# Performance work log

Measured on AMD Instinct MI355X. Metric: run time of the kernel, lower is better.

Reference implementation:

```python
import jax, jax.numpy as jnp
import numpy as np

K = 20
EPS = 1e-5  # BatchNorm eps
SLOPE = 0.2  # LeakyReLU negative slope


def _lrelu(y):
    return jnp.where(y > 0, y, SLOPE * y)


def _knn_idx(x):
    # x: [B, C, N] -> idx [B, N, K] of nearest neighbors (largest of negative sq dist)
    inner = -2.0 * jnp.einsum('bcn,bcm->bnm', x, x)
    xx = jnp.sum(x * x, axis=1)  # [B, N]
    pd = -xx[:, :, None] - inner - xx[:, None, :]  # [B, N, N]
    return jax.lax.top_k(pd, K)[1]


def _graph_feature(x):
    # x: [B, C, N] -> [B, 2C, N, K] = cat(neighbor - center, center)
    idx = _knn_idx(x)
    xt = jnp.transpose(x, (0, 2, 1))  # [B, N, C]
    nb = jax.vmap(lambda f, i: f[i])(xt, idx)  # [B, N, K, C]
    ctr = xt[:, :, None, :]
    feat = jnp.concatenate([nb - ctr, jnp.broadcast_to(ctr, nb.shape)], axis=-1)
    return jnp.transpose(feat, (0, 3, 1, 2))


def _bn(y, p, ch_axis):
    g, b, m, v = p[0], p[1], p[2], p[3]
    shape = [1] * y.ndim
    shape[ch_axis] = -1
    scale = (g / jnp.sqrt(v + EPS)).reshape(shape)
    return (y - m.reshape(shape)) * scale + b.reshape(shape)


def _conv_block(x, w, bn):
    f = _graph_feature(x)  # [B, 2C_in, N, K]
    y = jnp.einsum('bcnk,oc->bonk', f, w)  # 1x1 conv, no bias
    y = _lrelu(_bn(y, bn, 1))
    return jnp.max(y, axis=-1)  # max over K neighbors -> [B, C_out, N]


def setup_inputs() -> dict:
    key = jax.random.key(0)
    ks = jax.random.split(key, 20)
    B, N = 8, 1024
    inp = {
        'x': jax.random.normal(ks[0], (B, 3, N), jnp.float32),
        'w0': jax.random.normal(ks[1], (64, 6), jnp.float32) * 0.1,
        'w1': jax.random.normal(ks[2], (64, 128), jnp.float32) * 0.1,
        'w2': jax.random.normal(ks[3], (128, 128), jnp.float32) * 0.1,
        'w3': jax.random.normal(ks[4], (256, 256), jnp.float32) * 0.1,
        'bn0': jax.random.uniform(ks[5], (4, 64), jnp.float32) + 0.1,
        'bn1': jax.random.uniform(ks[6], (4, 64), jnp.float32) + 0.1,
        'bn2': jax.random.uniform(ks[7], (4, 128), jnp.float32) + 0.1,
        'bn3': jax.random.uniform(ks[8], (4, 256), jnp.float32) + 0.1,
        'we': jax.random.normal(ks[9], (1024, 512), jnp.float32) * 0.05,
        'bne': jax.random.uniform(ks[10], (4, 1024), jnp.float32) + 0.1,
        'wf0': jax.random.normal(ks[11], (512, 2048), jnp.float32) * 0.02,
        'bnf0': jax.random.uniform(ks[12], (4, 512), jnp.float32) + 0.1,
        'wf1': jax.random.normal(ks[13], (256, 512), jnp.float32) * 0.05,
        'bnf1': jax.random.uniform(ks[14], (4, 256), jnp.float32) + 0.1,
        'wfin': jax.random.normal(ks[15], (64, 256), jnp.float32) * 0.05,
        'bfin': jax.random.normal(ks[16], (64,), jnp.float32) * 0.05,
    }
    return inp


def reference(x, w0, w1, w2, w3, bn0, bn1, bn2, bn3, we, bne, wf0, bnf0, wf1, bnf1, wfin, bfin):
    B = x.shape[0]
    x1 = _conv_block(x, w0, bn0)   # [B, 64, N]
    x2 = _conv_block(x1, w1, bn1)  # [B, 64, N]
    x3 = _conv_block(x2, w2, bn2)  # [B, 128, N]
    x4 = _conv_block(x3, w3, bn3)  # [B, 256, N]
    cat = jnp.concatenate([x1, x2, x3, x4], axis=1)  # [B, 512, N]
    e = _lrelu(_bn(jnp.einsum('bcn,oc->bon', cat, we), bne, 1))  # [B, 1024, N]
    p1 = jnp.max(e, axis=-1)
    p2 = jnp.mean(e, axis=-1)
    h = jnp.concatenate([p1, p2], axis=1)  # [B, 2048]
    h = _lrelu(_bn(h @ wf0.T, bnf0, 1))  # [B, 512]; dropout is eval-mode identity
    h = _lrelu(_bn(h @ wf1.T, bnf1, 1))  # [B, 256]
    return h @ wfin.T + bfin  # [B, 64]
```

## Files before the change

kernel.cpp:

```cpp
#include <hip/hip_runtime.h>
#include <math.h>

#define N_PTS 1024
#define BATCH 8
#define KNN 20
#define EPSB 1e-5f
#define SLOPE 0.2f

typedef __attribute__((ext_vector_type(8))) short short8;
typedef __attribute__((ext_vector_type(4))) float f32x4;
typedef unsigned short ushort_t;
typedef unsigned long long u64;

#define LDS_U32(p) ((__attribute__((address_space(3))) unsigned int*)(p))
#define GLB_U32(p) ((const __attribute__((address_space(1))) unsigned int*)(p))

__device__ __forceinline__ void glds16(const ushort_t* g, ushort_t* l) {
    __builtin_amdgcn_global_load_lds(GLB_U32(g), LDS_U32(l), 16, 0, 0);
}

__device__ __forceinline__ float lrelu(float y) { return y > 0.f ? y : SLOPE * y; }

__device__ __forceinline__ ushort_t f2bf(float f) {
    union { float f; unsigned u; } v; v.f = f;
    unsigned r = v.u + 0x7FFF + ((v.u >> 16) & 1);
    return (ushort_t)(r >> 16);
}
__device__ __forceinline__ float bf2f(ushort_t h) {
    union { unsigned u; float f; } v; v.u = ((unsigned)h) << 16; return v.f;
}

__device__ __forceinline__ void wprep_one(const float* __restrict__ w, float* __restrict__ wpt,
                                          int C, int Cout, int g) {
    int M2 = 2 * Cout;
    if (g >= C * M2) return;
    int c = g / M2, m = g - c * M2;
    float v;
    if (m < Cout) v = w[(size_t)m * 2 * C + c];
    else { int o = m - Cout; v = w[(size_t)o * 2 * C + C + c] - w[(size_t)o * 2 * C + c]; }
    wpt[(size_t)c * M2 + m] = v;
}

__device__ __forceinline__ void wext_one(const float* __restrict__ w, ushort_t* __restrict__ Wext,
                                         int C, int Cout, int g, int lg2C) {
    int M2 = 2 * Cout;
    if (g >= C * M2) return;
    int m = g >> lg2C, c = g & (C - 1);
    float v;
    if (m < Cout) v = w[(size_t)m * 2 * C + c];
    else { int o = m - Cout; v = w[(size_t)o * 2 * C + C + c] - w[(size_t)o * 2 * C + c]; }
    ushort_t h = f2bf(v);
    float r1 = v - bf2f(h);
    ushort_t md = f2bf(r1);
    ushort_t lo = f2bf(r1 - bf2f(md));
    ushort_t* dst = Wext + (size_t)m * 3 * C + c;
    dst[0] = h; dst[C] = md; dst[2 * C] = lo;
}

__global__ void prep_kernel(const float* __restrict__ we, ushort_t* __restrict__ weh,
                            const float* __restrict__ w0, float* __restrict__ wpt0,
                            const float* __restrict__ w1, ushort_t* __restrict__ Wext1,
                            const float* __restrict__ w2, ushort_t* __restrict__ Wext2,
                            const float* __restrict__ w3, ushort_t* __restrict__ Wext3) {
    int bx = blockIdx.x, tid = threadIdx.x;
    if (bx < 512) {
        int g = bx * 256 + tid;
        float4 v = ((const float4*)we)[g];
        ushort4 o;
        o.x = f2bf(v.x); o.y = f2bf(v.y); o.z = f2bf(v.z); o.w = f2bf(v.w);
        ((ushort4*)weh)[g] = o;
    } else if (bx < 514) {
        wprep_one(w0, wpt0, 3, 64, (bx - 512) * 256 + tid);
    } else if (bx < 546) {
        wext_one(w1, Wext1, 64, 64, (bx - 514) * 256 + tid, 6);
    } else if (bx < 610) {
        wext_one(w2, Wext2, 64, 128, (bx - 546) * 256 + tid, 6);
    } else {
        wext_one(w3, Wext3, 128, 256, (bx - 610) * 256 + tid, 7);
    }
}

__global__ void __launch_bounds__(256)
split_kernel(const float* __restrict__ in, ushort_t* __restrict__ xT3,
             float* __restrict__ xxv, int C, int bstride) {
    int b = blockIdx.z, nt = blockIdx.x;
    int tid = threadIdx.x;
    __shared__ float tile[64][65];
    const float* ib = in + (size_t)b * bstride;
    int S3 = 3 * C;
    float xxa = 0.f;
    for (int ct = 0; ct < C; ct += 64) {
        __syncthreads();
        for (int qq = 0; qq < 16; qq++) {
            int e = qq * 256 + tid;
            int c = e >> 6, n = e & 63;
            tile[c][n] = ib[(size_t)(ct + c) * N_PTS + nt * 64 + n];
        }
        __syncthreads();
        if (tid < 64) {
            for (int c = 0; c < 64; c++) { float v = tile[c][tid]; xxa += v * v; }
        }
        for (int qq = 0; qq < 16; qq++) {
            int e = qq * 256 + tid;
            int n = e >> 6, c = e & 63;
            float v = tile[c][n];
            ushort_t h = f2bf(v);
            float r1 = v - bf2f(h);
            ushort_t md = f2bf(r1);
            ushort_t lo = f2bf(r1 - bf2f(md));
            ushort_t* dst = xT3 + ((size_t)b * N_PTS + nt * 64 + n) * S3 + ct + c;
            dst[0] = h; dst[C] = md; dst[2 * C] = lo;
        }
    }
    if (tid < 64) xxv[b * N_PTS + nt * 64 + tid] = xxa;
}

__global__ void __launch_bounds__(256)
pdabv_mfma(const ushort_t* __restrict__ xT3, const ushort_t* __restrict__ Wext,
           const float* __restrict__ xxv,
           float* __restrict__ pd, float* __restrict__ A, float* __restrict__ Bv,
           int C, int lg2C, int Cout) {
    int b = blockIdx.z, mt = blockIdx.y, nt = blockIdx.x;
    int tid = threadIdx.x;
    int wv = tid >> 6, lane = tid & 63, q = lane >> 4, lr = lane & 15;
    int mblk = wv >> 1, nblk = wv & 1;
    int srow = lane >> 2;
    int scol = (lane & 3) * 8;
    const int S3 = 3 * C;
    bool isPd = (mt < 8);
    const ushort_t* Abase = isPd ? (xT3 + ((size_t)b * N_PTS + mt * 128) * S3)
                                 : (Wext + (size_t)(mt - 8) * 128 * S3);
    const ushort_t* Bbase = xT3 + ((size_t)b * N_PTS + nt * 128) * S3;
    __shared__ __align__(16) ushort_t sA[128 * 32];
    __shared__ __align__(16) ushort_t sB[128 * 32];
    __shared__ float sxxA[128], sxxB[128];
    if (isPd && tid < 128) {
        sxxA[tid] = xxv[b * N_PTS + mt * 128 + tid];
        sxxB[tid] = xxv[b * N_PTS + nt * 128 + tid];
    }
    f32x4 acc[4][4] = {};
    const int pA6[6] = {0, 0, 1, 1, 0, 2};
    const int pB6[6] = {0, 1, 0, 1, 2, 0};
    const int pA3[3] = {0, 0, 1};
    const int pB3[3] = {0, 1, 0};
    int nseg = isPd ? 6 : 3;
    for (int ks = 0; ks < nseg * C; ks += 32) {
        int seg = ks >> lg2C;
        int kl = ks & (C - 1);
        int aoff = (isPd ? pA6[seg] : pA3[seg]) * C + kl;
        int boff = (isPd ? pB6[seg] : pB3[seg]) * C + kl;
        __syncthreads();
        #pragma unroll
        for (int h = 0; h < 2; h++) {
            int chunk = wv + h * 4;
            int row = chunk * 16 + srow;
            glds16(Abase + (size_t)row * S3 + aoff + scol, sA + chunk * 512);
            glds16(Bbase + (size_t)row * S3 + boff + scol, sB + chunk * 512);
        }
        __syncthreads();
        short8 af[4], bfr[4];
        for (int mi = 0; mi < 4; mi++)
            af[mi] = *(const short8*)&sA[(mblk * 64 + mi * 16 + lr) * 32 + q * 8];
        for (int ni = 0; ni < 4; ni++)
            bfr[ni] = *(const short8*)&sB[(nblk * 64 + ni * 16 + lr) * 32 + q * 8];
        for (int mi = 0; mi < 4; mi++)
            for (int ni = 0; ni < 4; ni++)
                acc[mi][ni] = __builtin_amdgcn_mfma_f32_16x16x32_bf16(af[mi], bfr[ni], acc[mi][ni], 0, 0, 0);
    }
    if (isPd) {
        for (int mi = 0; mi < 4; mi++)
        for (int r = 0; r < 4; r++) {
            int row = mblk * 64 + mi * 16 + q * 4 + r;
            float xr = sxxA[row];
            float* prow = pd + ((size_t)(b * N_PTS + mt * 128 + row)) * N_PTS + nt * 128;
            for (int ni = 0; ni < 4; ni++) {
                int col = nblk * 64 + ni * 16 + lr;
                prow[col] = 2.f * acc[mi][ni][r] - xr - sxxB[col];
            }
        }
    } else {
        for (int mi = 0; mi < 4; mi++)
        for (int r = 0; r < 4; r++) {
            int rowm = (mt - 8) * 128 + mblk * 64 + mi * 16 + q * 4 + r;
            float* dst = (rowm < Cout) ? (A + ((size_t)b * Cout + rowm) * N_PTS)
                                       : (Bv + ((size_t)b * Cout + rowm - Cout) * N_PTS);
            for (int ni = 0; ni < 4; ni++) {
                int col = nblk * 64 + ni * 16 + lr;
                dst[nt * 128 + col] = acc[mi][ni][r];
            }
        }
    }
}

__global__ void __launch_bounds__(256)
pdabv_valu(const float* __restrict__ x, const float* __restrict__ wpt,
           float* __restrict__ pd, float* __restrict__ A, float* __restrict__ Bv,
           int C, int Cout, int bstride) {
    int b = blockIdx.z;
    int nt = blockIdx.y;
    int bx = blockIdx.x;
    int tid = threadIdx.x;
    int tx = tid & 15, ty = tid >> 4;
    int n0 = nt * 128;
    __shared__ float sU0[16][128];
    __shared__ float sU1[16][128];
    __shared__ float sXX[256];
    const float* xb = x + (size_t)b * bstride;
    float acc[8][8] = {};
    if (bx < 8) {
        int m0 = bx * 128;
        float xxa = 0.f;
        for (int c0 = 0; c0 < C; c0 += 16) {
            for (int q = 0; q < 2; q++) {
                int f = q * 256 + tid;
                int r = f >> 5, col = (f & 31) * 4;
                int c = c0 + r;
                float4 vn = {0.f, 0.f, 0.f, 0.f}, vm = {0.f, 0.f, 0.f, 0.f};
                if (c < C) {
                    vn = *(const float4*)&xb[(size_t)c * N_PTS + n0 + col];
                    vm = *(const float4*)&xb[(size_t)c * N_PTS + m0 + col];
                }
                *(float4*)&sU0[r][col] = vn;
                *(float4*)&sU1[r][col] = vm;
            }
            __syncthreads();
            if (tid < 128) {
                for (int k = 0; k < 16; k++) { float v = sU0[k][tid]; xxa += v * v; }
            } else {
                int u = tid - 128;
                for (int k = 0; k < 16; k++) { float v = sU1[k][u]; xxa += v * v; }
            }
            for (int k = 0; k < 16; k++) {
                float4 a0 = *(const float4*)&sU0[k][ty * 4];
                float4 a1 = *(const float4*)&sU0[k][64 + ty * 4];
                float4 b0 = *(const float4*)&sU1[k][tx * 4];
                float4 b1 = *(const float4*)&sU1[k][64 + tx * 4];
                float av[8] = {a0.x, a0.y, a0.z, a0.w, a1.x, a1.y, a1.z, a1.w};
                float bw[8] = {b0.x, b0.y, b0.z, b0.w, b1.x, b1.y, b1.z, b1.w};
                for (int i = 0; i < 8; i++)
                    for (int j = 0; j < 8; j++) acc[i][j] += av[i] * bw[j];
            }
            __syncthreads();
        }
        sXX[tid] = xxa;
        __syncthreads();
        float xnv[8], xmv[8];
        for (int i = 0; i < 8; i++) xnv[i] = sXX[(i >> 2) * 64 + ty * 4 + (i & 3)];
        for (int j = 0; j < 8; j++) xmv[j] = sXX[128 + (j >> 2) * 64 + tx * 4 + (j & 3)];
        for (int i = 0; i < 8; i++) {
            int n = n0 + (i >> 2) * 64 + ty * 4 + (i & 3);
            float* prow = pd + ((size_t)(b * N_PTS + n)) * N_PTS;
            for (int jh = 0; jh < 2; jh++) {
                float4 o;
                o.x = 2.f * acc[i][jh * 4 + 0] - xnv[i] - xmv[jh * 4 + 0];
                o.y = 2.f * acc[i][jh * 4 + 1] - xnv[i] - xmv[jh * 4 + 1];
                o.z = 2.f * acc[i][jh * 4 + 2] - xnv[i] - xmv[jh * 4 + 2];
                o.w = 2.f * acc[i][jh * 4 + 3] - xnv[i] - xmv[jh * 4 + 3];
                *(float4*)&prow[m0 + jh * 64 + tx * 4] = o;
            }
        }
    } else {
        int m0 = (bx - 8) * 128;
        int M2 = 2 * Cout;
        for (int c0 = 0; c0 < C; c0 += 16) {
            for (int q = 0; q < 2; q++) {
                int f = q * 256 + tid;
                int r = f >> 5, col = (f & 31) * 4;
                int c = c0 + r;
                float4 vw = {0.f, 0.f, 0.f, 0.f}, vx = {0.f, 0.f, 0.f, 0.f};
                if (c < C) {
                    vw = *(const float4*)&wpt[(size_t)c * M2 + m0 + col];
                    vx = *(const float4*)&xb[(size_t)c * N_PTS + n0 + col];
                }
                *(float4*)&sU0[r][col] = vw;
                *(float4*)&sU1[r][col] = vx;
            }
            __syncthreads();
            for (int k = 0; k < 16; k++) {
                float4 a0 = *(const float4*)&sU0[k][ty * 4];
                float4 a1 = *(const float4*)&sU0[k][64 + ty * 4];
                float4 b0 = *(const float4*)&sU1[k][tx * 4];
                float4 b1 = *(const float4*)&sU1[k][64 + tx * 4];
                float av[8] = {a0.x, a0.y, a0.z, a0.w, a1.x, a1.y, a1.z, a1.w};
                float bw[8] = {b0.x, b0.y, b0.z, b0.w, b1.x, b1.y, b1.z, b1.w};
                for (int i = 0; i < 8; i++)
                    for (int j = 0; j < 8; j++) acc[i][j] += av[i] * bw[j];
            }
            __syncthreads();
        }
        for (int i = 0; i < 8; i++) {
            int rowm = m0 + (i >> 2) * 64 + ty * 4 + (i & 3);
            float* dst = (rowm < Cout) ? (A + ((size_t)b * Cout + rowm) * N_PTS)
                                       : (Bv + ((size_t)b * Cout + rowm - Cout) * N_PTS);
            for (int jh = 0; jh < 2; jh++) {
                float4 o;
                o.x = acc[i][jh * 4 + 0];
                o.y = acc[i][jh * 4 + 1];
                o.z = acc[i][jh * 4 + 2];
                o.w = acc[i][jh * 4 + 3];
                *(float4*)&dst[n0 + jh * 64 + tx * 4] = o;
            }
        }
    }
}

__global__ void __launch_bounds__(256)
topk_kernel(const float* __restrict__ pd, int* __restrict__ idx) {
    int wid = threadIdx.x >> 6;
    int row = blockIdx.x * 4 + wid;
    int lane = threadIdx.x & 63;
    __shared__ u64 Sk[4][64];
    const float* p = pd + (size_t)row * N_PTS;
    float v[16];
    for (int q = 0; q < 4; q++) {
        float4 t = *(const float4*)&p[lane * 16 + q * 4];
        v[q * 4 + 0] = t.x; v[q * 4 + 1] = t.y; v[q * 4 + 2] = t.z; v[q * 4 + 3] = t.w;
    }
    float lmax = v[0];
    #pragma unroll
    for (int j = 1; j < 16; j++) lmax = fmaxf(lmax, v[j]);
    float s = lmax;
    #pragma unroll
    for (int k = 2; k <= 64; k <<= 1) {
        #pragma unroll
        for (int j = k >> 1; j > 0; j >>= 1) {
            float o = __shfl_xor(s, j, 64);
            bool takeMin = (((lane & k) == 0) == ((lane & j) == 0));
            float mn = fminf(s, o), mx = fmaxf(s, o);
            s = takeMin ? mn : mx;
        }
    }
    float tp = __shfl(s, 44, 64);
    unsigned hm = 0;
    #pragma unroll
    for (int j = 0; j < 16; j++) hm |= (v[j] >= tp ? 1u : 0u) << j;
    int cnt = __popc(hm);
    int incl = cnt;
    #pragma unroll
    for (int d = 1; d < 64; d <<= 1) {
        int o = __shfl_up(incl, d, 64);
        if (lane >= d) incl += o;
    }
    int total = __shfl(incl, 63, 64);
    int pos = incl - cnt;
    if (total <= 64) {
        #pragma unroll
        for (int j = 0; j < 16; j++) {
            if (hm & (1u << j)) {
                unsigned u = __float_as_uint(v[j]);
                unsigned msk = ((unsigned)((int)u >> 31)) | 0x80000000u;
                Sk[wid][pos] = ((u64)(u ^ msk) << 32) | (unsigned)(1023 - (lane * 16 + j));
                pos++;
            }
        }
        u64 key = (lane < total) ? Sk[wid][lane] : 0ull;
        #pragma unroll
        for (int k = 2; k <= 64; k <<= 1) {
            #pragma unroll
            for (int j = k >> 1; j > 0; j >>= 1) {
                u64 o = __shfl_xor(key, j, 64);
                bool takeMin = (((lane & k) == 0) == ((lane & j) == 0));
                bool sgt = key > o;
                key = (sgt != takeMin) ? key : o;
            }
        }
        if (lane >= 44) {
            int m = 1023 - (int)(unsigned)(key & 0xFFFFFFFFu);
            idx[row * KNN + (63 - lane)] = m;
        }
    } else {
        for (int kk = 0; kk < KNN; kk++) {
            float bv = v[0]; int bj = 0;
            #pragma unroll
            for (int j = 1; j < 16; j++) if (v[j] > bv) { bv = v[j]; bj = j; }
            int bi = lane * 16 + bj;
            for (int d = 32; d > 0; d >>= 1) {
                float ov = __shfl_down(bv, d, 64);
                int oi = __shfl_down(bi, d, 64);
                if (ov > bv || (ov == bv && oi < bi)) { bv = ov; bi = oi; }
            }
            bi = __shfl(bi, 0, 64);
            if ((bi >> 4) == lane) {
                #pragma unroll
                for (int j = 0; j < 16; j++) if (j == (bi & 15)) v[j] = -INFINITY;
            }
            if (lane == 0) idx[row * KNN + kk] = bi;
        }
    }
}

__global__ void __launch_bounds__(256)
gmax_kernel(const float* __restrict__ A, const float* __restrict__ Bv,
            const int* __restrict__ idx, const float* __restrict__ bnp,
            float* __restrict__ out, int Cout, int outStrideB) {
    int b = blockIdx.z;
    int n0 = blockIdx.x * 64;
    int o0 = blockIdx.y * 4;
    int tid = threadIdx.x;
    __shared__ int sidx[64 * 21];
    __shared__ float sA[4][N_PTS];
    for (int t = tid; t < 64 * KNN; t += 256) {
        int nl = t / KNN, k = t - nl * KNN;
        sidx[nl * 21 + k] = idx[(b * N_PTS + n0) * KNN + t];
    }
    const float* Abase = A + ((size_t)b * Cout + o0) * N_PTS;
    for (int q = 0; q < 4; q++) {
        int f = q * 256 + tid;
        int r = f >> 8, c4 = (f & 255) * 4;
        *(float4*)&sA[r][c4] = *(const float4*)&Abase[(size_t)r * N_PTS + c4];
    }
    __syncthreads();
    int nl = tid & 63, ol = tid >> 6;
    float best = -INFINITY;
    #pragma unroll
    for (int k = 0; k < KNN; k++) {
        int j = sidx[nl * 21 + k];
        best = fmaxf(best, sA[ol][j]);
    }
    int o = o0 + ol;
    int n = n0 + nl;
    float pre = best + Bv[((size_t)b * Cout + o) * N_PTS + n];
    float g = bnp[o], bb = bnp[Cout + o], m = bnp[2 * Cout + o], vv = bnp[3 * Cout + o];
    float scale = g / sqrtf(vv + EPSB);
    out[(size_t)b * outStrideB + (size_t)o * N_PTS + n] = lrelu((pre - m) * scale + bb);
}

__global__ void catT_kernel(const float* __restrict__ cat, ushort_t* __restrict__ catT) {
    int b = blockIdx.z, ct = blockIdx.y, nt = blockIdx.x;
    int tid = threadIdx.x;
    __shared__ float tile[64][65];
    const float* cb = cat + (size_t)b * 512 * N_PTS;
    for (int q = 0; q < 16; q++) {
        int e = q * 256 + tid;
        int c = e >> 6, n = e & 63;
        tile[c][n] = cb[(size_t)(ct * 64 + c) * N_PTS + nt * 64 + n];
    }
    __syncthreads();
    for (int q = 0; q < 16; q++) {
        int e = q * 256 + tid;
        int n = e >> 6, c = e & 63;
        catT[((size_t)b * N_PTS + nt * 64 + n) * 512 + ct * 64 + c] = f2bf(tile[c][n]);
    }
}

__global__ void __launch_bounds__(256)
gemm6_mfma(const ushort_t* __restrict__ weh, const ushort_t* __restrict__ catT,
           const float* __restrict__ bne,
           float* __restrict__ pmax, float* __restrict__ psum) {
    int b = blockIdx.z, ot = blockIdx.y, nt = blockIdx.x;
    int tid = threadIdx.x;
    int wv = tid >> 6, lane = tid & 63, q = lane >> 4, lr = lane & 15;
    int mblk = wv >> 1, nblk = wv & 1;
    int srow = lane >> 2, scol = (lane & 3) * 8;
    __shared__ __align__(16) ushort_t sA[128 * 32];
    __shared__ __align__(16) ushort_t sB[128 * 32];
    __shared__ float sa[128], sc[128];
    __shared__ float redmax[128][2], redsum[128][2];
    int o0 = ot * 128, n0 = nt * 128;
    if (tid < 128) {
        int o = o0 + tid;
        float g = bne[o], bb = bne[1024 + o], m = bne[2048 + o], vv = bne[3072 + o];
        float scale = g / sqrtf(vv + EPSB);
        sa[tid] = scale; sc[tid] = bb - m * scale;
    }
    f32x4 acc[4][4] = {};
    const ushort_t* cT = catT + (size_t)b * N_PTS * 512;
    for (int k0 = 0; k0 < 512; k0 += 32) {
        __syncthreads();
        #pragma unroll
        for (int h = 0; h < 2; h++) {
            int chunk = wv + h * 4;
            int row = chunk * 16 + srow;
            glds16(weh + (size_t)(o0 + row) * 512 + k0 + scol, sA + chunk * 512);
            glds16(cT  + (size_t)(n0 + row) * 512 + k0 + scol, sB + chunk * 512);
        }
        __syncthreads();
        short8 af[4], bfr[4];
        for (int mi = 0; mi < 4; mi++)
            af[mi] = *(const short8*)&sA[(mblk * 64 + mi * 16 + lr) * 32 + q * 8];
        for (int ni = 0; ni < 4; ni++)
            bfr[ni] = *(const short8*)&sB[(nblk * 64 + ni * 16 + lr) * 32 + q * 8];
        for (int mi = 0; mi < 4; mi++)
            for (int ni = 0; ni < 4; ni++)
                acc[mi][ni] = __builtin_amdgcn_mfma_f32_16x16x32_bf16(af[mi], bfr[ni], acc[mi][ni], 0, 0, 0);
    }
    for (int mi = 0; mi < 4; mi++) {
        for (int r = 0; r < 4; r++) {
            int row = mblk * 64 + mi * 16 + q * 4 + r;
            float a = sa[row], c = sc[row];
            float mx = -INFINITY, sm = 0.f;
            for (int ni = 0; ni < 4; ni++) {
                float y = lrelu(acc[mi][ni][r] * a + c);
                mx = fmaxf(mx, y); sm += y;
            }
            for (int msk = 1; msk < 16; msk <<= 1) {
                mx = fmaxf(mx, __shfl_xor(mx, msk, 16));
                sm += __shfl_xor(sm, msk, 16);
            }
            if (lr == 0) { redmax[row][nblk] = mx; redsum[row][nblk] = sm; }
        }
    }
    __syncthreads();
    if (tid < 128) {
        float mx = fmaxf(redmax[tid][0], redmax[tid][1]);
        float sm = redsum[tid][0] + redsum[tid][1];
        int o = o0 + tid;
        pmax[((size_t)(b * 1024 + o)) * 8 + nt] = mx;
        psum[((size_t)(b * 1024 + o)) * 8 + nt] = sm;
    }
}

__global__ void pool_reduce_kernel(const float* __restrict__ pmax, const float* __restrict__ psum,
                                   float* __restrict__ h0) {
    int g = blockIdx.x * 256 + threadIdx.x;
    int b = g >> 10, o = g & 1023;
    float mx = -INFINITY, sm = 0.f;
    for (int t = 0; t < 8; t++) { mx = fmaxf(mx, pmax[g * 8 + t]); sm += psum[g * 8 + t]; }
    h0[(size_t)b * 2048 + o] = mx;
    h0[(size_t)b * 2048 + 1024 + o] = sm * (1.0f / 1024.0f);
}

__global__ void fc_kernel(const float* __restrict__ in, const float* __restrict__ w,
                          const float* __restrict__ bnp, const float* __restrict__ bias,
                          float* __restrict__ out, int Cin, int Cout, int mode) {
    int blk = blockIdx.x;
    int b = blk / Cout, o = blk % Cout;
    int lane = threadIdx.x;
    const float* inb = in + (size_t)b * Cin;
    const float* wo = w + (size_t)o * Cin;
    float acc = 0.f;
    for (int c = lane; c < Cin; c += 64) acc += inb[c] * wo[c];
    for (int s = 32; s > 0; s >>= 1) acc += __shfl_down(acc, s, 64);
    if (lane == 0) {
        float y = acc;
        if (mode == 0) {
            float g = bnp[o], bb = bnp[Cout + o], m = bnp[2 * Cout + o], vv = bnp[3 * Cout + o];
            y = lrelu((y - m) * (g / sqrtf(vv + EPSB)) + bb);
        } else {
            y += bias[o];
        }
        out[(size_t)b * Cout + o] = y;
    }
}

extern "C" void kernel_launch(void* const* d_in, const int* in_sizes, int n_in,
                              void* d_out, int out_size, void* d_ws, size_t ws_size,
                              hipStream_t stream) {
    const float* x    = (const float*)d_in[0];
    const float* w0   = (const float*)d_in[1];
    const float* w1   = (const float*)d_in[2];
    const float* w2   = (const float*)d_in[3];
    const float* w3   = (const float*)d_in[4];
    const float* bn0  = (const float*)d_in[5];
    const float* bn1  = (const float*)d_in[6];
    const float* bn2  = (const float*)d_in[7];
    const float* bn3  = (const float*)d_in[8];
    const float* we   = (const float*)d_in[9];
    const float* bne  = (const float*)d_in[10];
    const float* wf0  = (const float*)d_in[11];
    const float* bnf0 = (const float*)d_in[12];
    const float* wf1  = (const float*)d_in[13];
    const float* bnf1 = (const float*)d_in[14];
    const float* wfin = (const float*)d_in[15];
    const float* bfin = (const float*)d_in[16];

    float* ws = (float*)d_ws;
    size_t off = 0;
    float* cat  = ws + off; off += (size_t)BATCH * 512 * N_PTS;
    float* pd   = ws + off; off += (size_t)BATCH * N_PTS * N_PTS;
    float* A    = ws + off; off += (size_t)BATCH * 256 * N_PTS;
    float* Bv   = ws + off; off += (size_t)BATCH * 256 * N_PTS;
    float* pmax = ws + off; off += (size_t)BATCH * N_PTS * 8;
    float* psum = ws + off; off += (size_t)BATCH * N_PTS * 8;
    float* h0   = ws + off; off += (size_t)BATCH * 2048;
    float* h1   = ws + off; off += (size_t)BATCH * 512;
    float* h2   = ws + off; off += (size_t)BATCH * 256;
    float* xxv  = ws + off; off += (size_t)BATCH * N_PTS;
    int*   idx  = (int*)(ws + off); off += (size_t)BATCH * N_PTS * KNN;
    ushort_t* weh  = (ushort_t*)(ws + off); off += (size_t)(1024 * 512) / 2;
    ushort_t* catT = (ushort_t*)(ws + off); off += (size_t)BATCH * N_PTS * 512 / 2;
    ushort_t* xT3  = (ushort_t*)(ws + off); off += (size_t)BATCH * N_PTS * 3 * 128 / 2;
    ushort_t* Wext1 = (ushort_t*)(ws + off); off += (size_t)(128 * 3 * 64) / 2;
    ushort_t* Wext2 = (ushort_t*)(ws + off); off += (size_t)(256 * 3 * 64) / 2;
    ushort_t* Wext3 = (ushort_t*)(ws + off); off += (size_t)(512 * 3 * 128) / 2;
    float* wpt0 = ws + off; off += 3 * 128;

    const int CSTR = 512 * N_PTS;
    const int topkBlocks = BATCH * N_PTS / 4;

    prep_kernel<<<866, 256, 0, stream>>>(we, weh, w0, wpt0, w1, Wext1, w2, Wext2, w3, Wext3);

    pdabv_valu<<<dim3(9, 8, BATCH), 256, 0, stream>>>(x, wpt0, pd, A, Bv, 3, 64, 3 * N_PTS);
    topk_kernel<<<topkBlocks, 256, 0, stream>>>(pd, idx);
    gmax_kernel<<<dim3(16, 16, BATCH), 256, 0, stream>>>(A, Bv, idx, bn0, cat, 64, CSTR);

    split_kernel<<<dim3(16, 1, BATCH), 256, 0, stream>>>(cat, xT3, xxv, 64, CSTR);
    pdabv_mfma<<<dim3(8, 9, BATCH), 256, 0, stream>>>(xT3, Wext1, xxv, pd, A, Bv, 64, 6, 64);
    topk_kernel<<<topkBlocks, 256, 0, stream>>>(pd, idx);
    gmax_kernel<<<dim3(16, 16, BATCH), 256, 0, stream>>>(A, Bv, idx, bn1, cat + 64 * N_PTS, 64, CSTR);

    split_kernel<<<dim3(16, 1, BATCH), 256, 0, stream>>>(cat + 64 * N_PTS, xT3, xxv, 64, CSTR);
    pdabv_mfma<<<dim3(8, 10, BATCH), 256, 0, stream>>>(xT3, Wext2, xxv, pd, A, Bv, 64, 6, 128);
    topk_kernel<<<topkBlocks, 256, 0, stream>>>(pd, idx);
    gmax_kernel<<<dim3(16, 32, BATCH), 256, 0, stream>>>(A, Bv, idx, bn2, cat + 128 * N_PTS, 128, CSTR);

    split_kernel<<<dim3(16, 1, BATCH), 256, 0, stream>>>(cat + 128 * N_PTS, xT3, xxv, 128, CSTR);
    pdabv_mfma<<<dim3(8, 12, BATCH), 256, 0, stream>>>(xT3, Wext3, xxv, pd, A, Bv, 128, 7, 256);
    topk_kernel<<<topkBlocks, 256, 0, stream>>>(pd, idx);
    gmax_kernel<<<dim3(16, 64, BATCH), 256, 0, stream>>>(A, Bv, idx, bn3, cat + 256 * N_PTS, 256, CSTR);

    catT_kernel<<<dim3(16, 8, BATCH), 256, 0, stream>>>(cat, catT);
    gemm6_mfma<<<dim3(8, 8, BATCH), 256, 0, stream>>>(weh, catT, bne, pmax, psum);
    pool_reduce_kernel<<<32, 256, 0, stream>>>(pmax, psum, h0);

    fc_kernel<<<BATCH * 512, 64, 0, stream>>>(h0, wf0, bnf0, nullptr, h1, 2048, 512, 0);
    fc_kernel<<<BATCH * 256, 64, 0, stream>>>(h1, wf1, bnf1, nullptr, h2, 512, 256, 0);
    fc_kernel<<<BATCH * 64, 64, 0, stream>>>(h2, wfin, nullptr, bfin, (float*)d_out, 256, 64, 1);
}
```

Baseline: 338.8 us.

## Fuse pairwise-distance GEMM with top-k selection, keeping distance rows in LDS

Distances are now computed into shared memory for 16 query rows per block, and top-k runs on those rows directly. This removes the 32 MB pd matrix write and read for each of the four layers. The A/B projection GEMMs move to separate kernels. The fused kernel uses 64 KB of LDS per block and only 512 blocks per layer, with a small 16-row MFMA tile that rereads B tiles per block, so occupancy and GEMM efficiency may drop.

```diff
diff --git a/kernel.cpp b/kernel.cpp
--- a/kernel.cpp
+++ b/kernel.cpp
@@ -28,6 +28,85 @@
 }
 __device__ __forceinline__ float bf2f(ushort_t h) {
     union { unsigned u; float f; } v; v.u = ((unsigned)h) << 16; return v.f;
+}
+
+__device__ __forceinline__ void topk_row(const float* drow, int lane, u64* SkW,
+                                         int* idxout) {
+    float v[16];
+    #pragma unroll
+    for (int j = 0; j < 16; j++) v[j] = drow[j * 64 + lane];
+    float lmax = v[0];
+    #pragma unroll
+    for (int j = 1; j < 16; j++) lmax = fmaxf(lmax, v[j]);
+    float s = lmax;
+    #pragma unroll
+    for (int k = 2; k <= 64; k <<= 1) {
+        #pragma unroll
+        for (int j = k >> 1; j > 0; j >>= 1) {
+            float o = __shfl_xor(s, j, 64);
+            bool takeMin = (((lane & k) == 0) == ((lane & j) == 0));
+            float mn = fminf(s, o), mx = fmaxf(s, o);
+            s = takeMin ? mn : mx;
+        }
+    }
+    float tp = __shfl(s, 44, 64);
+    unsigned hm = 0;
+    #pragma unroll
+    for (int j = 0; j < 16; j++) hm |= (v[j] >= tp ? 1u : 0u) << j;
+    int cnt = __popc(hm);
+    int incl = cnt;
+    #pragma unroll
+    for (int d = 1; d < 64; d <<= 1) {
+        int o = __shfl_up(incl, d, 64);
+        if (lane >= d) incl += o;
+    }
+    int total = __shfl(incl, 63, 64);
+    int pos = incl - cnt;
+    if (total <= 64) {
+        #pragma unroll
+        for (int j = 0; j < 16; j++) {
+            if (hm & (1u << j)) {
+                unsigned u = __float_as_uint(v[j]);
+                unsigned msk = ((unsigned)((int)u >> 31)) | 0x80000000u;
+                int e = j * 64 + lane;
+                SkW[pos] = ((u64)(u ^ msk) << 32) | (unsigned)(1023 - e);
+                pos++;
+            }
+        }
+        u64 key = (lane < total) ? SkW[lane] : 0ull;
+        #pragma unroll
+        for (int k = 2; k <= 64; k <<= 1) {
+            #pragma unroll
+            for (int j = k >> 1; j > 0; j >>= 1) {
+                u64 o = __shfl_xor(key, j, 64);
+                bool takeMin = (((lane & k) == 0) == ((lane & j) == 0));
+                bool sgt = key > o;
+                key = (sgt != takeMin) ? key : o;
+            }
+        }
+        if (lane >= 44) {
+            int m = 1023 - (int)(unsigned)(key & 0xFFFFFFFFu);
+            idxout[63 - lane] = m;
+        }
+    } else {
+        for (int kk = 0; kk < KNN; kk++) {
+            float bv = v[0]; int bj = 0;
+            #pragma unroll
+            for (int j = 1; j < 16; j++) if (v[j] > bv) { bv = v[j]; bj = j; }
+            int bi = bj * 64 + lane;
+            for (int d = 32; d > 0; d >>= 1) {
+                float ov = __shfl_down(bv, d, 64);
+                int oi = __shfl_down(bi, d, 64);
+                if (ov > bv || (ov == bv && oi < bi)) { bv = ov; bi = oi; }
+            }
+            bi = __shfl(bi, 0, 64);
+            if ((bi & 63) == lane) {
+                #pragma unroll
+                for (int j = 0; j < 16; j++) if (j == (bi >> 6)) v[j] = -INFINITY;
+            }
+            if (lane == 0) idxout[kk] = bi;
+        }
+    }
 }
 
 __device__ __forceinline__ void wprep_one(const float* __restrict__ w, float* __restrict__ wpt,
@@ -116,39 +195,128 @@
 }
 
 __global__ void __launch_bounds__(256)
-pdabv_mfma(const ushort_t* __restrict__ xT3, const ushort_t* __restrict__ Wext,
-           const float* __restrict__ xxv,
-           float* __restrict__ pd, float* __restrict__ A, float* __restrict__ Bv,
-           int C, int lg2C, int Cout) {
+pdtopk_mfma(const ushort_t* __restrict__ xT3, const float* __restrict__ xxv,
+            int* __restrict__ idx, int C, int lg2C) {
+    int b = blockIdx.y;
+    int n0 = blockIdx.x * 16;
+    int tid = threadIdx.x;
+    int wv = tid >> 6, lane = tid & 63, q = lane >> 4, lr = lane & 15;
+    int srow = lane >> 2, scol = (lane & 3) * 8;
+    const int S3 = 3 * C;
+    __shared__ float dist[16 * 1024];
+    __shared__ __align__(16) ushort_t sB[128 * 32];
+    __shared__ u64 Sk[4][64];
+    const ushort_t* Abase = xT3 + ((size_t)b * N_PTS + n0) * S3;
+    const int pA6[6] = {0, 0, 1, 1, 0, 2};
+    const int pB6[6] = {0, 1, 0, 1, 2, 0};
+    for (int mt = 0; mt < 8; mt++) {
+        const ushort_t* Bbase = xT3 + ((size_t)b * N_PTS + mt * 128) * S3;
+        f32x4 acc[2] = {};
+        for (int ks = 0; ks < 6 * C; ks += 32) {
+            int seg = ks >> lg2C;
+            int kl = ks & (C - 1);
+            int aoff = pA6[seg] * C + kl, boff = pB6[seg] * C + kl;
+            __syncthreads();
+            #pragma unroll
+            for (int h = 0; h < 2; h++) {
+                int chunk = wv + h * 4;
+                int row = chunk * 16 + srow;
+                glds16(Bbase + (size_t)row * S3 + boff + scol, sB + chunk * 512);
+            }
+            short8 af = *(const short8*)(Abase + (size_t)lr * S3 + aoff + q * 8);
+            __syncthreads();
+            #pragma unroll
+            for (int j = 0; j < 2; j++) {
+                int cb = wv * 2 + j;
+                short8 bf = *(const short8*)&sB[(cb * 16 + lr) * 32 + q * 8];
+                acc[j] = __builtin_amdgcn_mfma_f32_16x16x32_bf16(af, bf, acc[j], 0, 0, 0);
+            }
+        }
+        #pragma unroll
+        for (int j = 0; j < 2; j++) {
+            int col = mt * 128 + (wv * 2 + j) * 16 + lr;
+            float xm = xxv[b * N_PTS + col];
+            #pragma unroll
+            for (int r = 0; r < 4; r++) {
+                int row = q * 4 + r;
+                float xn = xxv[b * N_PTS + n0 + row];
+                dist[row * 1024 + col] = 2.f * acc[j][r] - xn - xm;
+            }
+        }
+    }
+    __syncthreads();
+    for (int rr = 0; rr < 4; rr++) {
+        int row = wv * 4 + rr;
+        topk_row(&dist[row * 1024], lane, Sk[wv], idx + ((size_t)(b * N_PTS + n0 + row)) * KNN);
+    }
+}
+
+__global__ void __launch_bounds__(256)
+pdtopk_valu(const float* __restrict__ x, int* __restrict__ idx, int bstride) {
+    int b = blockIdx.y;
+    int n0 = blockIdx.x * 16;
+    int tid = threadIdx.x;
+    int wv = tid >> 6, lane = tid & 63;
+    __shared__ float dist[16 * 1024];
+    __shared__ float sx[3][N_PTS];
+    __shared__ float sxxn[16];
+    __shared__ u64 Sk[4][64];
+    const float* xb = x + (size_t)b * bstride;
+    for (int t = tid; t < 3 * N_PTS; t += 256) {
+        int c = t >> 10, m = t & 1023;
+        sx[c][m] = xb[c * N_PTS + m];
+    }
+    __syncthreads();
+    if (tid < 16) {
+        int n = n0 + tid;
+        float s = sx[0][n] * sx[0][n] + sx[1][n] * sx[1][n] + sx[2][n] * sx[2][n];
+        sxxn[tid] = s;
+    }
+    float xs0[4], xs1[4], xs2[4], xxm[4];
+    #pragma unroll
+    for (int t = 0; t < 4; t++) {
+        int m = tid + t * 256;
+        xs0[t] = sx[0][m]; xs1[t] = sx[1][m]; xs2[t] = sx[2][m];
+        xxm[t] = xs0[t] * xs0[t] + xs1[t] * xs1[t] + xs2[t] * xs2[t];
+    }
+    __syncthreads();
+    for (int r = 0; r < 16; r++) {
+        float xn0 = sx[0][n0 + r], xn1 = sx[1][n0 + r], xn2 = sx[2][n0 + r];
+        float xxn = sxxn[r];
+        #pragma unroll
+        for (int t = 0; t < 4; t++) {
+            int m = tid + t * 256;
+            float dot = xn0 * xs0[t] + xn1 * xs1[t] + xn2 * xs2[t];
+            dist[r * 1024 + m] = 2.f * dot - xxn - xxm[t];
+        }
+    }
+    __syncthreads();
+    for (int rr = 0; rr < 4; rr++) {
+        int row = wv * 4 + rr;
+        topk_row(&dist[row * 1024], lane, Sk[wv], idx + ((size_t)(b * N_PTS + n0 + row)) * KNN);
+    }
+}
+
+__global__ void __launch_bounds__(256)
+abv_mfma(const ushort_t* __restrict__ xT3, const ushort_t* __restrict__ Wext,
+         float* __restrict__ A, float* __restrict__ Bv, int C, int lg2C, int Cout) {
     int b = blockIdx.z, mt = blockIdx.y, nt = blockIdx.x;
     int tid = threadIdx.x;
     int wv = tid >> 6, lane = tid & 63, q = lane >> 4, lr = lane & 15;
     int mblk = wv >> 1, nblk = wv & 1;
-    int srow = lane >> 2;
-    int scol = (lane & 3) * 8;
+    int srow = lane >> 2, scol = (lane & 3) * 8;
     const int S3 = 3 * C;
-    bool isPd = (mt < 8);
-    const ushort_t* Abase = isPd ? (xT3 + ((size_t)b * N_PTS + mt * 128) * S3)
-                                 : (Wext + (size_t)(mt - 8) * 128 * S3);
+    const ushort_t* Abase = Wext + (size_t)mt * 128 * S3;
     const ushort_t* Bbase = xT3 + ((size_t)b * N_PTS + nt * 128) * S3;
     __shared__ __align__(16) ushort_t sA[128 * 32];
     __shared__ __align__(16) ushort_t sB[128 * 32];
-    __shared__ float sxxA[128], sxxB[128];
-    if (isPd && tid < 128) {
-        sxxA[tid] = xxv[b * N_PTS + mt * 128 + tid];
-        sxxB[tid] = xxv[b * N_PTS + nt * 128 + tid];
-    }
     f32x4 acc[4][4] = {};
-    const int pA6[6] = {0, 0, 1, 1, 0, 2};
-    const int pB6[6] = {0, 1, 0, 1, 2, 0};
     const int pA3[3] = {0, 0, 1};
     const int pB3[3] = {0, 1, 0};
-    int nseg = isPd ? 6 : 3;
-    for (int ks = 0; ks < nseg * C; ks += 32) {
+    for (int ks = 0; ks < 3 * C; ks += 32) {
         int seg = ks >> lg2C;
         int kl = ks & (C - 1);
-        int aoff = (isPd ? pA6[seg] : pA3[seg]) * C + kl;
-        int boff = (isPd ? pB6[seg] : pB3[seg]) * C + kl;
+        int aoff = pA3[seg] * C + kl, boff = pB3[seg] * C + kl;
         __syncthreads();
         #pragma unroll
         for (int h = 0; h < 2; h++) {
@@ -167,224 +335,70 @@
             for (int ni = 0; ni < 4; ni++)
                 acc[mi][ni] = __builtin_amdgcn_mfma_f32_16x16x32_bf16(af[mi], bfr[ni], acc[mi][ni], 0, 0, 0);
     }
-    if (isPd) {
-        for (int mi = 0; mi < 4; mi++)
-        for (int r = 0; r < 4; r++) {
-            int row = mblk * 64 + mi * 16 + q * 4 + r;
-            float xr = sxxA[row];
-            float* prow = pd + ((size_t)(b * N_PTS + mt * 128 + row)) * N_PTS + nt * 128;
-            for (int ni = 0; ni < 4; ni++) {
-                int col = nblk * 64 + ni * 16 + lr;
-                prow[col] = 2.f * acc[mi][ni][r] - xr - sxxB[col];
-            }
-        }
-    } else {
-        for (int mi = 0; mi < 4; mi++)
-        for (int r = 0; r < 4; r++) {
-            int rowm = (mt - 8) * 128 + mblk * 64 + mi * 16 + q * 4 + r;
-            float* dst = (rowm < Cout) ? (A + ((size_t)b * Cout + rowm) * N_PTS)
-                                       : (Bv + ((size_t)b * Cout + rowm - Cout) * N_PTS);
-            for (int ni = 0; ni < 4; ni++) {
-                int col = nblk * 64 + ni * 16 + lr;
-                dst[nt * 128 + col] = acc[mi][ni][r];
-            }
+    for (int mi = 0; mi < 4; mi++)
+    for (int r = 0; r < 4; r++) {
+        int rowm = mt * 128 + mblk * 64 + mi * 16 + q * 4 + r;
+        float* dst = (rowm < Cout) ? (A + ((size_t)b * Cout + rowm) * N_PTS)
+                                   : (Bv + ((size_t)b * Cout + rowm - Cout) * N_PTS);
+        for (int ni = 0; ni < 4; ni++) {
+            int col = nblk * 64 + ni * 16 + lr;
+            dst[nt * 128 + col] = acc[mi][ni][r];
         }
     }
 }
 
 __global__ void __launch_bounds__(256)
-pdabv_valu(const float* __restrict__ x, const float* __restrict__ wpt,
-           float* __restrict__ pd, float* __restrict__ A, float* __restrict__ Bv,
-           int C, int Cout, int bstride) {
+abv_valu(const float* __restrict__ x, const float* __restrict__ wpt,
+         float* __restrict__ A, float* __restrict__ Bv,
+         int C, int Cout, int bstride) {
     int b = blockIdx.z;
-    int nt = blockIdx.y;
-    int bx = blockIdx.x;
+    int nt = blockIdx.x;
+    int m0 = blockIdx.y * 128;
     int tid = threadIdx.x;
     int tx = tid & 15, ty = tid >> 4;
     int n0 = nt * 128;
+    int M2 = 2 * Cout;
     __shared__ float sU0[16][128];
     __shared__ float sU1[16][128];
-    __shared__ float sXX[256];
     const float* xb = x + (size_t)b * bstride;
     float acc[8][8] = {};
-    if (bx < 8) {
-        int m0 = bx * 128;
-        float xxa = 0.f;
-        for (int c0 = 0; c0 < C; c0 += 16) {
-            for (int q = 0; q < 2; q++) {
-                int f = q * 256 + tid;
-                int r = f >> 5, col = (f & 31) * 4;
-                int c = c0 + r;
-                float4 vn = {0.f, 0.f, 0.f, 0.f}, vm = {0.f, 0.f, 0.f, 0.f};
-                if (c < C) {
-                    vn = *(const float4*)&xb[(size_t)c * N_PTS + n0 + col];
-                    vm = *(const float4*)&xb[(size_t)c * N_PTS + m0 + col];
-                }
-                *(float4*)&sU0[r][col] = vn;
-                *(float4*)&sU1[r][col] = vm;
-            }
-            __syncthreads();
-            if (tid < 128) {
-                for (int k = 0; k < 16; k++) { float v = sU0[k][tid]; xxa += v * v; }
-            } else {
-                int u = tid - 128;
-                for (int k = 0; k < 16; k++) { float v = sU1[k][u]; xxa += v * v; }
-            }
-            for (int k = 0; k < 16; k++) {
-                float4 a0 = *(const float4*)&sU0[k][ty * 4];
-                float4 a1 = *(const float4*)&sU0[k][64 + ty * 4];
-                float4 b0 = *(const float4*)&sU1[k][tx * 4];
-                float4 b1 = *(const float4*)&sU1[k][64 + tx * 4];
-                float av[8] = {a0.x, a0.y, a0.z, a0.w, a1.x, a1.y, a1.z, a1.w};
-                float bw[8] = {b0.x, b0.y, b0.z, b0.w, b1.x, b1.y, b1.z, b1.w};
-                for (int i = 0; i < 8; i++)
-                    for (int j = 0; j < 8; j++) acc[i][j] += av[i] * bw[j];
-            }
-            __syncthreads();
-        }
-        sXX[tid] = xxa;
-        __syncthreads();
-        float xnv[8], xmv[8];
-        for (int i = 0; i < 8; i++) xnv[i] = sXX[(i >> 2) * 64 + ty * 4 + (i & 3)];
-        for (int j = 0; j < 8; j++) xmv[j] = sXX[128 + (j >> 2) * 64 + tx * 4 + (j & 3)];
-        for (int i = 0; i < 8; i++) {
-            int n = n0 + (i >> 2) * 64 + ty * 4 + (i & 3);
-            float* prow = pd + ((size_t)(b * N_PTS + n)) * N_PTS;
-            for (int jh = 0; jh < 2; jh++) {
-                float4 o;
-                o.x = 2.f * acc[i][jh * 4 + 0] - xnv[i] - xmv[jh * 4 + 0];
-                o.y = 2.f * acc[i][jh * 4 + 1] - xnv[i] - xmv[jh * 4 + 1];
-                o.z = 2.f * acc[i][jh * 4 + 2] - xnv[i] - xmv[jh * 4 + 2];
-                o.w = 2.f * acc[i][jh * 4 + 3] - xnv[i] - xmv[jh * 4 + 3];
-                *(float4*)&prow[m0 + jh * 64 + tx * 4] = o;
-            }
-        }
-    } else {
-        int m0 = (bx - 8) * 128;
-        int M2 = 2 * Cout;
-        for (int c0 = 0; c0 < C; c0 += 16) {
-            for (int q = 0; q < 2; q++) {
-                int f = q * 256 + tid;
-                int r = f >> 5, col = (f & 31) * 4;
-                int c = c0 + r;
-                float4 vw = {0.f, 0.f, 0.f, 0.f}, vx = {0.f, 0.f, 0.f, 0.f};
-                if (c < C) {
-                    vw = *(const float4*)&wpt[(size_t)c * M2 + m0 + col];
-                    vx = *(const float4*)&xb[(size_t)c * N_PTS + n0 + col];
-                }
-                *(float4*)&sU0[r][col] = vw;
-                *(float4*)&sU1[r][col] = vx;
-            }
-            __syncthreads();
-            for (int k = 0; k < 16; k++) {
-                float4 a0 = *(const float4*)&sU0[k][ty * 4];
-                float4 a1 = *(const float4*)&sU0[k][64 + ty * 4];
-                float4 b0 = *(const float4*)&sU1[k][tx * 4];
-                float4 b1 = *(const float4*)&sU1[k][64 + tx * 4];
-                float av[8] = {a0.x, a0.y, a0.z, a0.w, a1.x, a1.y, a1.z, a1.w};
-                float bw[8] = {b0.x, b0.y, b0.z, b0.w, b1.x, b1.y, b1.z, b1.w};
-                for (int i = 0; i < 8; i++)
-                    for (int j = 0; j < 8; j++) acc[i][j] += av[i] * bw[j];
-            }
-            __syncthreads();
-        }
-        for (int i = 0; i < 8; i++) {
-            int rowm = m0 + (i >> 2) * 64 + ty * 4 + (i & 3);
-            float* dst = (rowm < Cout) ? (A + ((size_t)b * Cout + rowm) * N_PTS)
-                                       : (Bv + ((size_t)b * Cout + rowm - Cout) * N_PTS);
-            for (int jh = 0; jh < 2; jh++) {
-                float4 o;
-                o.x = acc[i][jh * 4 + 0];
-                o.y = acc[i][jh * 4 + 1];
-                o.z = acc[i][jh * 4 + 2];
-                o.w = acc[i][jh * 4 + 3];
-                *(float4*)&dst[n0 + jh * 64 + tx * 4] = o;
-            }
-        }
-    }
-}
-
-__global__ void __launch_bounds__(256)
-topk_kernel(const float* __restrict__ pd, int* __restrict__ idx) {
-    int wid = threadIdx.x >> 6;
-    int row = blockIdx.x * 4 + wid;
-    int lane = threadIdx.x & 63;
-    __shared__ u64 Sk[4][64];
-    const float* p = pd + (size_t)row * N_PTS;
-    float v[16];
-    for (int q = 0; q < 4; q++) {
-        float4 t = *(const float4*)&p[lane * 16 + q * 4];
-        v[q * 4 + 0] = t.x; v[q * 4 + 1] = t.y; v[q * 4 + 2] = t.z; v[q * 4 + 3] = t.w;
-    }
-    float lmax = v[0];
-    #pragma unroll
-    for (int j = 1; j < 16; j++) lmax = fmaxf(lmax, v[j]);
-    float s = lmax;
-    #pragma unroll
-    for (int k = 2; k <= 64; k <<= 1) {
-        #pragma unroll
-        for (int j = k >> 1; j > 0; j >>= 1) {
-            float o = __shfl_xor(s, j, 64);
-            bool takeMin = (((lane & k) == 0) == ((lane & j) == 0));
-            float mn = fminf(s, o), mx = fmaxf(s, o);
-            s = takeMin ? mn : mx;
-        }
-    }
-    float tp = __shfl(s, 44, 64);
-    unsigned hm = 0;
-    #pragma unroll
-    for (int j = 0; j < 16; j++) hm |= (v[j] >= tp ? 1u : 0u) << j;
-    int cnt = __popc(hm);
-    int incl = cnt;
-    #pragma unroll
-    for (int d = 1; d < 64; d <<= 1) {
-        int o = __shfl_up(incl, d, 64);
-        if (lane >= d) incl += o;
-    }
-    int total = __shfl(incl, 63, 64);
-    int pos = incl - cnt;
-    if (total <= 64) {
-        #pragma unroll
-        for (int j = 0; j < 16; j++) {
-            if (hm & (1u << j)) {
-                unsigned u = __float_as_uint(v[j]);
-                unsigned msk = ((unsigned)((int)u >> 31)) | 0x80000000u;
-                Sk[wid][pos] = ((u64)(u ^ msk) << 32) | (unsigned)(1023 - (lane * 16 + j));
-                pos++;
-            }
-        }
-        u64 key = (lane < total) ? Sk[wid][lane] : 0ull;
-        #pragma unroll
-        for (int k = 2; k <= 64; k <<= 1) {
-            #pragma unroll
-            for (int j = k >> 1; j > 0; j >>= 1) {
-                u64 o = __shfl_xor(key, j, 64);
-                bool takeMin = (((lane & k) == 0) == ((lane & j) == 0));
-                bool sgt = key > o;
-                key = (sgt != takeMin) ? key : o;
-            }
-        }
-        if (lane >= 44) {
-            int m = 1023 - (int)(unsigned)(key & 0xFFFFFFFFu);
-            idx[row * KNN + (63 - lane)] = m;
-        }
-    } else {
-        for (int kk = 0; kk < KNN; kk++) {
-            float bv = v[0]; int bj = 0;
-            #pragma unroll
-            for (int j = 1; j < 16; j++) if (v[j] > bv) { bv = v[j]; bj = j; }
-            int bi = lane * 16 + bj;
-            for (int d = 32; d > 0; d >>= 1) {
-                float ov = __shfl_down(bv, d, 64);
-                int oi = __shfl_down(bi, d, 64);
-                if (ov > bv || (ov == bv && oi < bi)) { bv = ov; bi = oi; }
-            }
-            bi = __shfl(bi, 0, 64);
-            if ((bi >> 4) == lane) {
-                #pragma unroll
-                for (int j = 0; j < 16; j++) if (j == (bi & 15)) v[j] = -INFINITY;
-            }
-            if (lane == 0) idx[row * KNN + kk] = bi;
+    for (int c0 = 0; c0 < C; c0 += 16) {
+        for (int qq = 0; qq < 2; qq++) {
+            int f = qq * 256 + tid;
+            int r = f >> 5, col = (f & 31) * 4;
+            int c = c0 + r;
+            float4 vw = {0.f, 0.f, 0.f, 0.f}, vx = {0.f, 0.f, 0.f, 0.f};
+            if (c < C) {
+                vw = *(const float4*)&wpt[(size_t)c * M2 + m0 + col];
+                vx = *(const float4*)&xb[(size_t)c * N_PTS + n0 + col];
+            }
+            *(float4*)&sU0[r][col] = vw;
+            *(float4*)&sU1[r][col] = vx;
+        }
+        __syncthreads();
+        for (int k = 0; k < 16; k++) {
+            float4 a0 = *(const float4*)&sU0[k][ty * 4];
+            float4 a1 = *(const float4*)&sU0[k][64 + ty * 4];
+            float4 b0 = *(const float4*)&sU1[k][tx * 4];
+            float4 b1 = *(const float4*)&sU1[k][64 + tx * 4];
+            float av[8] = {a0.x, a0.y, a0.z, a0.w, a1.x, a1.y, a1.z, a1.w};
+            float bw[8] = {b0.x, b0.y, b0.z, b0.w, b1.x, b1.y, b1.z, b1.w};
+            for (int i = 0; i < 8; i++)
+                for (int j = 0; j < 8; j++) acc[i][j] += av[i] * bw[j];
+        }
+        __syncthreads();
+    }
+    for (int i = 0; i < 8; i++) {
+        int rowm = m0 + (i >> 2) * 64 + ty * 4 + (i & 3);
+        float* dst = (rowm < Cout) ? (A + ((size_t)b * Cout + rowm) * N_PTS)
+                                   : (Bv + ((size_t)b * Cout + rowm - Cout) * N_PTS);
+        for (int jh = 0; jh < 2; jh++) {
+            float4 o;
+            o.x = acc[i][jh * 4 + 0];
+            o.y = acc[i][jh * 4 + 1];
+            o.z = acc[i][jh * 4 + 2];
+            o.w = acc[i][jh * 4 + 3];
+            *(float4*)&dst[n0 + jh * 64 + tx * 4] = o;
         }
     }
 }
@@ -567,7 +581,6 @@
     float* ws = (float*)d_ws;
     size_t off = 0;
     float* cat  = ws + off; off += (size_t)BATCH * 512 * N_PTS;
-    float* pd   = ws + off; off += (size_t)BATCH * N_PTS * N_PTS;
     float* A    = ws + off; off += (size_t)BATCH * 256 * N_PTS;
     float* Bv   = ws + off; off += (size_t)BATCH * 256 * N_PTS;
     float* pmax = ws + off; off += (size_t)BATCH * N_PTS * 8;
@@ -586,33 +599,32 @@
     float* wpt0 = ws + off; off += 3 * 128;
 
     const int CSTR = 512 * N_PTS;
-    const int topkBlocks = BATCH * N_PTS / 4;
+    const dim3 pdtGrid(64, BATCH);
 
     prep_kernel<<<866, 256, 0, stream>>>(we, weh, w0, wpt0, w1, Wext1, w2, Wext2, w3, Wext3);
 
-    pdabv_valu<<<dim3(9, 8, BATCH), 256, 0, stream>>>(x, wpt0, pd, A, Bv, 3, 64, 3 * N_PTS);
-    topk_kernel<<<topkBlocks, 256, 0, stream>>>(pd, idx);
+    pdtopk_valu<<<pdtGrid, 256, 0, stream>>>(x, idx, 3 * N_PTS);
+    abv_valu<<<dim3(8, 1, BATCH), 256, 0, stream>>>(x, wpt0, A, Bv, 3, 64, 3 * N_PTS);
     gmax_kernel<<<dim3(16, 16, BATCH), 256, 0, stream>>>(A, Bv, idx, bn0, cat, 64, CSTR);
 
     split_kernel<<<dim3(16, 1, BATCH), 256, 0, stream>>>(cat, xT3, xxv, 64, CSTR);
-    pdabv_mfma<<<dim3(8, 9, BATCH), 256, 0, stream>>>(xT3, Wext1, xxv, pd, A, Bv, 64, 6, 64);
-    topk_kernel<<<topkBlocks, 256, 0, stream>>>(pd, idx);
+    pdtopk_mfma<<<pdtGrid, 256, 0, stream>>>(xT3, xxv, idx, 64, 6);
+    abv_mfma<<<dim3(8, 1, BATCH), 256, 0, stream>>>(xT3, Wext1, A, Bv, 64, 6, 64);
     gmax_kernel<<<dim3(16, 16, BATCH), 256, 0, stream>>>(A, Bv, idx, bn1, cat + 64 * N_PTS, 64, CSTR);
 
     split_kernel<<<dim3(16, 1, BATCH), 256, 0, stream>>>(cat + 64 * N_PTS, xT3, xxv, 64, CSTR);
-    pdabv_mfma<<<dim3(8, 10, BATCH), 256, 0, stream>>>(xT3, Wext2, xxv, pd, A, Bv, 64, 6, 128);
-    topk_kernel<<<topkBlocks, 256, 0, stream>>>(pd, idx);
+    pdtopk_mfma<<<pdtGrid, 256, 0, stream>>>(xT3, xxv, idx, 64, 6);
+    abv_mfma<<<dim3(8, 2, BATCH), 256, 0, stream>>>(xT3, Wext2, A, Bv, 64, 6, 128);
     gmax_kernel<<<dim3(16, 32, BATCH), 256, 0, stream>>>(A, Bv, idx, bn2, cat + 128 * N_PTS, 128, CSTR);
 
     split_kernel<<<dim3(16, 1, BATCH), 256, 0, stream>>>(cat + 128 * N_PTS, xT3, xxv, 128, CSTR);
-    pdabv_mfma<<<dim3(8, 12, BATCH), 256, 0, stream>>>(xT3, Wext3, xxv, pd, A, Bv, 128, 7, 256);
-    topk_kernel<<<topkBlocks, 256, 0, stream>>>(pd, idx);
+    pdtopk_mfma<<<pdtGrid, 256, 0, stream>>>(xT3, xxv, idx, 128, 7);
+    abv_mfma<<<dim3(8, 4, BATCH), 256, 0, stream>>>(xT3, Wext3, A, Bv, 128, 7, 256);
     gmax_kernel<<<dim3(16, 64, BATCH), 256, 0, stream>>>(A, Bv, idx, bn3, cat + 256 * N_PTS, 256, CSTR);
 
     catT_kernel<<<dim3(16, 8, BATCH), 256, 0, stream>>>(cat, catT);
     gemm6_mfma<<<dim3(8, 8, BATCH), 256, 0, stream>>>(weh, catT, bne, pmax, psum);
     pool_reduce_kernel<<<32, 256, 0, stream>>>(pmax, psum, h0);
-
     fc_kernel<<<BATCH * 512, 64, 0, stream>>>(h0, wf0, bnf0, nullptr, h1, 2048, 512, 0);
     fc_kernel<<<BATCH * 256, 64, 0, stream>>>(h1, wf1, bnf1, nullptr, h2, 512, 256, 0);
     fc_kernel<<<BATCH * 64, 64, 0, stream>>>(h2, wfin, nullptr, bfin, (float*)d_out, 256, 64, 1);
```

New measurement: 490.8 us. 1.45x slower.
